# Kernel optimization log

Hardware: AMD Instinct MI355X
Metric: run time of the kernel (lower is better)

The kernel has to match this reference:

```python
import jax, jax.numpy as jnp
import numpy as np

HEADS, DIM_HEAD, LANDMARKS, PINV_ITERS = 8, 64, 256, 6


def moore_penrose_pinv(x, iters=PINV_ITERS):
    abs_x = jnp.abs(x)
    col = abs_x.sum(-1)
    row = abs_x.sum(-2)
    z = jnp.swapaxes(x, -1, -2) / (jnp.max(col) * jnp.max(row))
    I = jnp.eye(x.shape[-1], dtype=x.dtype)
    for _ in range(iters):
        xz = x @ z
        z = 0.25 * z @ (13 * I - xz @ (15 * I - xz @ (7 * I - xz)))
    return z


def nystrom_attention(x, w_qkv, w_out, b_out, res_conv_w):
    b, n, dim = x.shape
    m = LANDMARKS
    pad = (m - n % m) % m
    x = jnp.pad(x, ((0, 0), (pad, 0), (0, 0)))  # pad at front like F.pad(x,(0,0,pad,0))
    npad = n + pad
    qkv = x @ w_qkv  # (b, npad, 3*heads*dim_head)
    q, k, v = jnp.split(qkv, 3, axis=-1)
    sh = lambda t: t.reshape(b, npad, HEADS, DIM_HEAD).transpose(0, 2, 1, 3)
    q, k, v = sh(q), sh(k), sh(v)  # (b,h,npad,dh)
    q = q * (DIM_HEAD ** -0.5)
    l = npad // m
    q_l = q.reshape(b, HEADS, m, l, DIM_HEAD).mean(axis=3)  # landmarks (b,h,m,dh)
    k_l = k.reshape(b, HEADS, m, l, DIM_HEAD).mean(axis=3)
    attn1 = jax.nn.softmax(jnp.einsum('bhid,bhjd->bhij', q, k_l), -1)   # (b,h,npad,m)
    attn2 = jax.nn.softmax(jnp.einsum('bhid,bhjd->bhij', q_l, k_l), -1)  # (b,h,m,m)
    attn3 = jax.nn.softmax(jnp.einsum('bhid,bhjd->bhij', q_l, k), -1)   # (b,h,m,npad)
    out = attn1 @ (moore_penrose_pinv(attn2) @ (attn3 @ v))  # (b,h,npad,dh)
    # depthwise residual conv over sequence dim (Conv2d(heads,heads,(33,1),groups=heads,bias=False))
    res = jax.lax.conv_general_dilated(v, res_conv_w, (1, 1), ((16, 16), (0, 0)),
                                       dimension_numbers=('NCHW', 'OIHW', 'NCHW'),
                                       feature_group_count=HEADS)
    out = out + res
    out = out.transpose(0, 2, 1, 3).reshape(b, npad, HEADS * DIM_HEAD)
    out = out @ w_out + b_out
    return out[:, -n:]


def camil_forward(bag, adj_row, adj_col, adj_val, w_qkv, w_out, b_out, res_conv_w,
                  wq, wk, wv_w, wv_b, v_att, u_att, w_att, fc_kernel, fc_bias):
    N = bag.shape[1]
    # encoder
    xg = nystrom_attention(bag, w_qkv, w_out, b_out, res_conv_w)[0]  # (N,D)
    enc = xg + bag  # (1,N,D)
    q = enc @ wq  # (1,N,256)
    k = enc @ wk
    attn = jnp.einsum('bnd,bmd->bnm', q, k)[0] / jnp.sqrt(jnp.float32(256.0))  # (N,N)
    # sparse adjacency-masked neighbor aggregation
    edge_scores = adj_val * attn[adj_row, adj_col]
    A_raw = jax.ops.segment_sum(edge_scores, adj_row, num_segments=N)  # (N,)
    alpha = jax.nn.softmax(A_raw)
    value = bag @ wv_w + wv_b  # (1,N,D)
    xl = alpha[:, None] * value  # (1,N,D)
    wei2 = jax.nn.sigmoid(-xl) ** 2
    xo = xl * 2 * wei2 + 2 * enc * (1 - wei2)  # (1,N,D)
    # gated MIL attention (softmax over dim 0 of size 1, as in original)
    inst = jnp.tanh(xo @ v_att) * jax.nn.sigmoid(xo @ u_att)
    scores = inst @ w_att  # (1,N,1)
    k_alpha = jax.nn.softmax(scores, axis=0)
    attn_output = k_alpha * xo
    pooled = attn_output[0].sum(axis=0, keepdims=True)  # (1,D)
    out = pooled @ fc_kernel + fc_bias  # (1,1)
    return out, A_raw, k_alpha


def setup_inputs() -> dict:
    key = jax.random.key(0)
    ks = jax.random.split(key, 16)
    N, D, E = 10000, 512, 90000
    s = 0.02
    return {
        'bag': jax.random.normal(ks[0], (1, N, D), jnp.float32),
        'adj_row': jax.random.randint(ks[1], (E,), 0, N),
        'adj_col': jax.random.randint(ks[2], (E,), 0, N),
        'adj_val': jax.random.uniform(ks[3], (E,), jnp.float32),
        'w_qkv': jax.random.normal(ks[4], (D, 3 * HEADS * DIM_HEAD), jnp.float32) * s,
        'w_out': jax.random.normal(ks[5], (HEADS * DIM_HEAD, D), jnp.float32) * s,
        'b_out': jnp.zeros((D,), jnp.float32),
        'res_conv_w': jax.random.normal(ks[6], (HEADS, 1, 33, 1), jnp.float32) * s,
        'wq': jax.random.normal(ks[7], (D, 256), jnp.float32) * s,
        'wk': jax.random.normal(ks[8], (D, 256), jnp.float32) * s,
        'wv_w': jax.random.normal(ks[9], (D, D), jnp.float32) * s,
        'wv_b': jnp.zeros((D,), jnp.float32),
        'v_att': jax.random.normal(ks[10], (D, 128), jnp.float32) * s,
        'u_att': jax.random.normal(ks[11], (D, 128), jnp.float32) * s,
        'w_att': jax.random.normal(ks[12], (128, 1), jnp.float32) * s,
        'fc_kernel': jax.random.normal(ks[13], (D, 1), jnp.float32) * s,
        'fc_bias': jnp.zeros((1,), jnp.float32),
    }


def reference(bag, adj_row, adj_col, adj_val, w_qkv, w_out, b_out, res_conv_w,
              wq, wk, wv_w, wv_b, v_att, u_att, w_att, fc_kernel, fc_bias):
    return camil_forward(bag, adj_row, adj_col, adj_val, w_qkv, w_out, b_out, res_conv_w,
                         wq, wk, wv_w, wv_b, v_att, u_att, w_att, fc_kernel, fc_bias)
```

## Files before the change

### kernel.cpp

```cpp
#include <hip/hip_runtime.h>
#include <hip/hip_bf16.h>
#include <math.h>

#define NSEQ   10000
#define NPAD   10240
#define PADR   240
#define HEADS  8
#define DH     64
#define LM     256
#define LFAC   40
#define DMODEL 512
#define DQK    256
#define OUTSZ  20001
#define NSPLIT 16
#define KCH    128

typedef __attribute__((ext_vector_type(8))) short bf16x8;
typedef __attribute__((ext_vector_type(4))) float f32x4;
#define MFMA16(a,b,c) __builtin_amdgcn_mfma_f32_16x16x32_bf16(a,b,c,0,0,0)

typedef __attribute__((address_space(1))) const unsigned char gconst_t;
typedef __attribute__((address_space(3))) unsigned char lds_t;
#define GLD16(gp, lp) __builtin_amdgcn_global_load_lds((gconst_t*)(gp), (lds_t*)(lp), 16, 0, 0)

__device__ __forceinline__ float b2f(ushort u) {
    return __uint_as_float(((unsigned)u) << 16);
}
__device__ __forceinline__ ushort f2b(float f) {
    unsigned u = __float_as_uint(f);
    unsigned r = (u + 0x7FFFu + ((u >> 16) & 1u)) >> 16;
    return (ushort)r;
}
__device__ __forceinline__ int swz8(int bid, int nwg) {
    int q = nwg >> 3, r = nwg & 7;
    int x = bid & 7, idx = bid >> 3;
    int start = (x < r) ? x * (q + 1) : r * (q + 1) + (x - r) * q;
    return start + idx;
}
__device__ __forceinline__ f32x4 tr4(f32x4 v, int p) {
    f32x4 u, w;
    float s, r;
    s = (p & 1) ? v[0] : v[1]; r = __shfl_xor(s, 1);
    u[0] = (p & 1) ? r : v[0]; u[1] = (p & 1) ? v[1] : r;
    s = (p & 1) ? v[2] : v[3]; r = __shfl_xor(s, 1);
    u[2] = (p & 1) ? r : v[2]; u[3] = (p & 1) ? v[3] : r;
    s = (p & 2) ? u[0] : u[2]; r = __shfl_xor(s, 2);
    w[0] = (p & 2) ? r : u[0]; w[2] = (p & 2) ? u[2] : r;
    s = (p & 2) ? u[1] : u[3]; r = __shfl_xor(s, 2);
    w[1] = (p & 2) ? r : u[1]; w[3] = (p & 2) ? u[3] : r;
    return w;
}

__global__ __launch_bounds__(256)
void cvt_k(const float* __restrict__ in, ushort* __restrict__ out, int n4,
           float* __restrict__ outbuf, const float* __restrict__ fcb,
           unsigned int* __restrict__ mx)
{
    int i = blockIdx.x * 256 + threadIdx.x;
    if (i < n4) {
        float4 v = ((const float4*)in)[i];
        ushort4 u; u.x = f2b(v.x); u.y = f2b(v.y); u.z = f2b(v.z); u.w = f2b(v.w);
        ((ushort4*)out)[i] = u;
    }
    if (i == 0) { outbuf[0] = fcb[0]; mx[0] = 0u; mx[1] = 0u; }
    if (i >= 1 && i <= NSEQ) outbuf[i] = 0.f;
    if (i >= NSEQ + 1 && i < OUTSZ) outbuf[i] = 1.0f;
}

__global__ __launch_bounds__(256)
void wtrans_k(const float* __restrict__ w_qkv, const float* __restrict__ w_out,
              const float* __restrict__ wq, const float* __restrict__ wk,
              const float* __restrict__ wv_w,
              ushort* __restrict__ wqkvT, ushort* __restrict__ woutT,
              ushort* __restrict__ wqkT)
{
    __shared__ float tile[32][33];
    int g0 = blockIdx.x * 32, r0 = blockIdx.y * 32;
    const float* in; ushort* outp; int C; int lc0;
    if (g0 < 1536)      { in = w_qkv; outp = wqkvT;                      C = 1536; lc0 = g0; }
    else if (g0 < 2048) { in = w_out; outp = woutT;                      C = 512;  lc0 = g0 - 1536; }
    else if (g0 < 2304) { in = wq;    outp = wqkT;                       C = 256;  lc0 = g0 - 2048; }
    else if (g0 < 2560) { in = wk;    outp = wqkT + 256*512;             C = 256;  lc0 = g0 - 2304; }
    else                { in = wv_w;  outp = wqkvT + (size_t)1536*512;   C = 512;  lc0 = g0 - 2560; }
    int tx = threadIdx.x & 31, ty = threadIdx.x >> 5;
    for (int i = ty; i < 32; i += 8) tile[i][tx] = in[(size_t)(r0 + i) * C + lc0 + tx];
    __syncthreads();
    for (int i = ty; i < 32; i += 8) outp[(size_t)(lc0 + i) * 512 + r0 + tx] = f2b(tile[tx][i]);
}

template<int MODE, int TN>
__global__ __launch_bounds__(256)
void mgemm(const ushort* __restrict__ A, const ushort* __restrict__ Bt,
           int Mlog, int N, int K, int padr, int nbx,
           void* __restrict__ P0, void* __restrict__ P1, void* __restrict__ P2,
           void* __restrict__ P3, void* __restrict__ P4,
           const float* __restrict__ bias, const float* __restrict__ extra)
{
    constexpr int NF = TN / 32;
    __shared__ __align__(16) char As[128 * 64];
    __shared__ __align__(16) char Bs[TN * 64];
    const int tid = threadIdx.x;
    const int l = tid & 63, w = tid >> 6;
    const int wm = w >> 1, wn = w & 1;
    const int wk_ = swz8(blockIdx.x, gridDim.x);
    const int row0 = (wk_ / nbx) * 128, col0 = (wk_ % nbx) * TN;
    const int lr = l & 15, lg = l >> 4;
    const bool slow = (MODE == 0) && (row0 < padr);
    f32x4 acc[4][NF];
    #pragma unroll
    for (int i = 0; i < 4; ++i)
        #pragma unroll
        for (int j = 0; j < NF; ++j) acc[i][j] = (f32x4){0.f, 0.f, 0.f, 0.f};

    for (int k0 = 0; k0 < K; k0 += 32) {
        if (!slow) {
            #pragma unroll
            for (int c = 0; c < 2; ++c) {
                int q = w * 2 + c;
                int row = q * 16 + (l >> 2);
                GLD16(A + (size_t)(row0 + row - padr) * K + k0 + (l & 3) * 8,
                      As + q * 1024);
            }
            if (TN == 128) {
                #pragma unroll
                for (int c = 0; c < 2; ++c) {
                    int q = w * 2 + c;
                    int row = q * 16 + (l >> 2);
                    GLD16(Bt + (size_t)(col0 + row) * K + k0 + (l & 3) * 8,
                          Bs + q * 1024);
                }
            } else {
                int row = w * 16 + (l >> 2);
                GLD16(Bt + (size_t)(col0 + row) * K + k0 + (l & 3) * 8,
                      Bs + w * 1024);
            }
        } else {
            #pragma unroll
            for (int c = 0; c < 2; ++c) {
                int gidx = c * 256 + tid;
                int row = gidx >> 2, gr = gidx & 3;
                int phys = row0 + row - padr;
                uint4 v = {0, 0, 0, 0};
                if (phys >= 0 && phys < Mlog - padr)
                    v = *(const uint4*)(A + (size_t)phys * K + k0 + gr * 8);
                *(uint4*)(As + gidx * 16) = v;
            }
            if (TN == 128) {
                #pragma unroll
                for (int c = 0; c < 2; ++c) {
                    int gidx = c * 256 + tid;
                    int row = gidx >> 2, gr = gidx & 3;
                    *(uint4*)(Bs + gidx * 16) =
                        *(const uint4*)(Bt + (size_t)(col0 + row) * K + k0 + gr * 8);
                }
            } else {
                int row = tid >> 2, gr = tid & 3;
                *(uint4*)(Bs + tid * 16) =
                    *(const uint4*)(Bt + (size_t)(col0 + row) * K + k0 + gr * 8);
            }
        }
        __syncthreads();
        bf16x8 af[4];
        #pragma unroll
        for (int mf = 0; mf < 4; ++mf)
            af[mf] = *(const bf16x8*)(As + (wm * 64 + mf * 16 + lr) * 64 + lg * 16);
        #pragma unroll
        for (int nf = 0; nf < NF; ++nf) {
            bf16x8 bfr = *(const bf16x8*)(Bs + (wn * (TN / 2) + nf * 16 + lr) * 64 + lg * 16);
            #pragma unroll
            for (int mf = 0; mf < 4; ++mf)
                acc[mf][nf] = MFMA16(af[mf], bfr, acc[mf][nf]);
        }
        __syncthreads();
    }

    const int p = lr & 3;
    #pragma unroll
    for (int mf = 0; mf < 4; ++mf)
    #pragma unroll
    for (int nf = 0; nf < NF; ++nf) {
        int cb   = col0 + wn * (TN / 2) + nf * 16 + (lr & 12);
        int rowT = row0 + wm * 64 + mf * 16 + lg * 4 + p;
        if (MODE == 0) {
            int c = col0 + wn * (TN / 2) + nf * 16 + lr;
            if ((c >> 9) == 2) {
                int hh = (c >> 6) & 7;
                int kt  = (row0 + wm * 64 + mf * 16 + lg * 4) >> 5;
                int lgp = ((mf * 2) + (lg >> 1)) & 3;
                int lanep = lr + lgp * 16;
                int e0 = (lg & 1) * 4;
                ushort4 pk;
                pk.x = f2b(acc[mf][nf][0]); pk.y = f2b(acc[mf][nf][1]);
                pk.z = f2b(acc[mf][nf][2]); pk.w = f2b(acc[mf][nf][3]);
                *(ushort4*)&((ushort*)P3)[(((size_t)hh * (NPAD/32) + kt) * 4 + (nf & 3)) * 512
                                          + lanep * 8 + e0] = pk;
            }
            int t = cb >> 9;
            f32x4 v = acc[mf][nf];
            if (t == 0) { v[0] *= 0.125f; v[1] *= 0.125f; v[2] *= 0.125f; v[3] *= 0.125f; }
            f32x4 wv = tr4(v, p);
            ushort4 pk;
            pk.x = f2b(wv[0]); pk.y = f2b(wv[1]); pk.z = f2b(wv[2]); pk.w = f2b(wv[3]);
            if (t < 3) {
                int hh = (cb >> 6) & 7, d0 = cb & 63;
                ushort* dst = (t == 0) ? (ushort*)P0 : (t == 1) ? (ushort*)P1 : (ushort*)P2;
                *(ushort4*)&dst[((size_t)hh * NPAD + rowT) * DH + d0] = pk;
            } else {
                int phys = rowT - PADR;
                if (phys >= 0)
                    *(ushort4*)&((ushort*)P4)[(size_t)phys * DMODEL + (cb & 511)] = pk;
            }
        } else if (MODE == 1) {
            f32x4 wv = tr4(acc[mf][nf], p);
            if (rowT < Mlog) {
                float4 bi = *(const float4*)(bias + cb);
                float4 ex = *(const float4*)(extra + (size_t)rowT * N + cb);
                float o0 = wv[0] + bi.x + ex.x, o1 = wv[1] + bi.y + ex.y;
                float o2 = wv[2] + bi.z + ex.z, o3 = wv[3] + bi.w + ex.w;
                *(float4*)&((float*)P0)[(size_t)rowT * N + cb] = make_float4(o0, o1, o2, o3);
                ushort4 pk; pk.x = f2b(o0); pk.y = f2b(o1); pk.z = f2b(o2); pk.w = f2b(o3);
                *(ushort4*)&((ushort*)P1)[(size_t)rowT * N + cb] = pk;
            }
        } else if (MODE == 6) {
            f32x4 wv = tr4(acc[mf][nf], p);
            if (rowT < Mlog) {
                ushort4 pk;
                pk.x = f2b(wv[0]); pk.y = f2b(wv[1]); pk.z = f2b(wv[2]); pk.w = f2b(wv[3]);
                if (cb < 256)
                    *(ushort4*)&((ushort*)P0)[(size_t)rowT * 256 + cb] = pk;
                else
                    *(ushort4*)&((ushort*)P1)[(size_t)rowT * 256 + (cb - 256)] = pk;
            }
        }
    }
}

template<bool PLAIN, bool BCI, bool WPK>
__global__ __launch_bounds__(256)
void pinv_k(const ushort* __restrict__ A, const ushort* __restrict__ Bt,
            int N, float cval, float scale,
            ushort* __restrict__ P0, ushort* __restrict__ P1)
{
    __shared__ __align__(16) char smem[49152];
    char* As = smem;
    char* Bs = smem + 16384;
    const int tid = threadIdx.x, l = tid & 63, w = tid >> 6;
    const int lr = l & 15, lg = l >> 4;
    const int col0 = blockIdx.x * 64, row0 = blockIdx.y * 32, h = blockIdx.z;
    const ushort* Ab = A + (size_t)h * 65536;
    const ushort* Btb = Bt + (size_t)h * ((size_t)N * 256);
    {
        int row = tid >> 3, seg = (tid & 7) * 64;
        const uint4* sa = (const uint4*)(Ab + (size_t)(row0 + row) * 256) + (tid & 7) * 4;
        #pragma unroll
        for (int e = 0; e < 4; ++e) {
            int off = (row * 512 + seg + e * 16) ^ ((row & 7) << 4);
            *(uint4*)(As + off) = sa[e];
        }
    }
    {
        int row = tid >> 2, seg = (tid & 3) * 128;
        const uint4* sb = (const uint4*)(Btb + (size_t)(col0 + row) * 256) + (tid & 3) * 8;
        int gn = col0 + row;
        #pragma unroll
        for (int e = 0; e < 8; ++e) {
            int off = (row * 512 + seg + e * 16) ^ ((row & 7) << 4);
            uint4 vb = sb[e];
            if (BCI) {
                union { uint4 u; ushort s[8]; } t; t.u = vb;
                int gk0 = (seg >> 1) + e * 8;
                #pragma unroll
                for (int j = 0; j < 8; ++j)
                    t.s[j] = f2b(((gn == gk0 + j) ? cval : 0.f) - b2f(t.s[j]));
                vb = t.u;
            }
            *(uint4*)(Bs + off) = vb;
        }
    }
    __syncthreads();
    f32x4 acc[2];
    acc[0] = (f32x4){0.f, 0.f, 0.f, 0.f};
    acc[1] = (f32x4){0.f, 0.f, 0.f, 0.f};
    #pragma unroll
    for (int ks = 0; ks < 8; ++ks) {
        bf16x8 af[2];
        #pragma unroll
        for (int mf = 0; mf < 2; ++mf) {
            int ar = mf * 16 + lr;
            af[mf] = *(const bf16x8*)(As + ((ar * 512 + ks * 64 + lg * 16) ^ ((ar & 7) << 4)));
        }
        int br = w * 16 + lr;
        bf16x8 bf = *(const bf16x8*)(Bs + ((br * 512 + ks * 64 + lg * 16) ^ ((br & 7) << 4)));
        acc[0] = MFMA16(af[0], bf, acc[0]);
        acc[1] = MFMA16(af[1], bf, acc[1]);
    }
    #pragma unroll
    for (int mf = 0; mf < 2; ++mf) {
        int r0v = row0 + mf * 16 + lg * 4;
        int c = col0 + w * 16 + lr;
        if (PLAIN) {
            #pragma unroll
            for (int i = 0; i < 4; ++i)
                P0[(size_t)h * 256 * N + (size_t)(r0v + i) * N + c] = f2b(acc[mf][i] * scale);
        }
        ushort4 pk;
        pk.x = f2b(acc[mf][0] * scale); pk.y = f2b(acc[mf][1] * scale);
        pk.z = f2b(acc[mf][2] * scale); pk.w = f2b(acc[mf][3] * scale);
        if (WPK) {
            int off = (((c >> 4) * 8 + (r0v >> 5)) << 9) + (((r0v >> 3) & 3) << 7)
                    + ((c & 15) << 3) + (r0v & 4);
            *(ushort4*)&P1[(size_t)h * 16384 + off] = pk;
        } else {
            *(ushort4*)&P1[(size_t)h * ((size_t)N * 256) + (size_t)c * 256 + r0v] = pk;
        }
    }
}

__global__ void landmark2_k(const ushort* __restrict__ Qb, const ushort* __restrict__ Kb,
                            ushort* __restrict__ QLb, ushort* __restrict__ KLb,
                            ushort* __restrict__ KLpk)
{
    int b = blockIdx.x;
    bool isK = b >= HEADS * LM;
    if (isK) b -= HEADS * LM;
    int hh = b >> 8, j = b & 255, d = threadIdx.x;
    const ushort* p = (isK ? Kb : Qb) + ((size_t)hh * NPAD + (size_t)j * LFAC) * DH + d;
    float s = 0.f;
    #pragma unroll
    for (int t = 0; t < LFAC; ++t) s += b2f(p[t * DH]);
    ushort u = f2b(s * (1.f / LFAC));
    (isK ? KLb : QLb)[((size_t)hh * LM + j) * DH + d] = u;
    if (isK) {
        int nf = j >> 4, lr = j & 15;
        int ks = d >> 5, lg = (d >> 3) & 3, e = d & 7;
        KLpk[(((size_t)hh * 16 + nf) * 2 + ks) * 512 + (lg * 16 + lr) * 8 + e] = u;
    }
}

__global__ __launch_bounds__(256)
void attn2_k(const ushort* __restrict__ QL, const ushort* __restrict__ KL,
             ushort* __restrict__ X2b)
{
    int i = blockIdx.x, h = blockIdx.y, j = threadIdx.x;
    __shared__ float qv[DH];
    __shared__ float red[256];
    if (j < DH) qv[j] = b2f(QL[((size_t)h * LM + i) * DH + j]);
    __syncthreads();
    const uint4* kp = (const uint4*)(KL + ((size_t)h * LM + j) * DH);
    float dot = 0.f;
    #pragma unroll
    for (int cc = 0; cc < 8; ++cc) {
        union { uint4 u; ushort s[8]; } uu; uu.u = kp[cc];
        #pragma unroll
        for (int e = 0; e < 8; ++e) dot += qv[cc * 8 + e] * b2f(uu.s[e]);
    }
    red[j] = dot; __syncthreads();
    for (int s = 128; s > 0; s >>= 1) { if (j < s) red[j] = fmaxf(red[j], red[j + s]); __syncthreads(); }
    float mx = red[0]; __syncthreads();
    float e = __expf(dot - mx);
    red[j] = e; __syncthreads();
    for (int s = 128; s > 0; s >>= 1) { if (j < s) red[j] += red[j + s]; __syncthreads(); }
    X2b[((size_t)h * LM + i) * LM + j] = f2b(e / red[0]);
}

__global__ __launch_bounds__(256)
void colrow_k(const ushort* __restrict__ X2b, unsigned int* __restrict__ mx)
{
    int h = blockIdx.x, t = threadIdx.x;
    const ushort* x = X2b + (size_t)h * LM * LM;
    float cs = 0.f, rs = 0.f;
    for (int j = 0; j < LM; ++j) cs += fabsf(b2f(x[(size_t)t * LM + j]));
    for (int i = 0; i < LM; ++i) rs += fabsf(b2f(x[(size_t)i * LM + t]));
    __shared__ float r1[256], r2[256];
    r1[t] = cs; r2[t] = rs; __syncthreads();
    for (int s = 128; s > 0; s >>= 1) {
        if (t < s) { r1[t] = fmaxf(r1[t], r1[t + s]); r2[t] = fmaxf(r2[t], r2[t + s]); }
        __syncthreads();
    }
    if (t == 0) {
        atomicMax(&mx[0], __float_as_uint(r1[0]));
        atomicMax(&mx[1], __float_as_uint(r2[0]));
    }
}

__global__ void zinit_k(const ushort* __restrict__ X2b, const float* __restrict__ mxf,
                        ushort* __restrict__ Z, ushort* __restrict__ Zt)
{
    int i = blockIdx.x, h = blockIdx.y, j = threadIdx.x;
    float scale = 1.f / (mxf[0] * mxf[1]);
    float x = b2f(X2b[((size_t)h * LM + i) * LM + j]) * scale;
    ushort u = f2b(x);
    Z[((size_t)h * LM + j) * LM + i] = u;
    Zt[((size_t)h * LM + i) * LM + j] = u;
}

__global__ __launch_bounds__(256)
void attn3_fa(const ushort* __restrict__ QLb, const ushort* __restrict__ Kb,
              const ushort* __restrict__ VtPk,
              float* __restrict__ Opart, float* __restrict__ Mpart,
              float* __restrict__ Lpart)
{
    __shared__ __align__(16) char smem[9216 + 18432];
    ushort* Qs = (ushort*)smem;
    ushort* Ks = (ushort*)(smem + 9216);
    ushort* Ps = (ushort*)(smem + 9216);
    const int tid = threadIdx.x, l = tid & 63, wv = tid >> 6;
    const int split = blockIdx.x, qt = blockIdx.y, h = blockIdx.z;
    const int lr = l & 15, lg = l >> 4;
    {
        int row = tid >> 2, seg = (tid & 3) * 16;
        const uint4* src = (const uint4*)(QLb + ((size_t)h * LM + qt * 64 + row) * DH + seg);
        *(uint4*)&Qs[row * 72 + seg] = src[0];
        *(uint4*)&Qs[row * 72 + seg + 8] = src[1];
    }
    f32x4 o[4];
    float m_[4], l_[4];
    #pragma unroll
    for (int nf = 0; nf < 4; ++nf) o[nf] = (f32x4){0.f, 0.f, 0.f, 0.f};
    #pragma unroll
    for (int i = 0; i < 4; ++i) { m_[i] = -INFINITY; l_[i] = 0.f; }
    const int k0base = split * (NPAD / NSPLIT);
    for (int ch = 0; ch < NPAD / NSPLIT / KCH; ++ch) {
        int kg0 = k0base + ch * KCH;
        __syncthreads();
        {
            int row = tid >> 1, half = (tid & 1) * 32;
            const uint4* src = (const uint4*)(Kb + ((size_t)h * NPAD + kg0 + row) * DH + half);
            #pragma unroll
            for (int e = 0; e < 4; ++e) *(uint4*)&Ks[row * 72 + half + e * 8] = src[e];
        }
        __syncthreads();
        f32x4 s[8];
        #pragma unroll
        for (int nf = 0; nf < 8; ++nf) s[nf] = (f32x4){0.f, 0.f, 0.f, 0.f};
        #pragma unroll
        for (int ks = 0; ks < 2; ++ks) {
            bf16x8 a = *(const bf16x8*)&Qs[(wv * 16 + lr) * 72 + ks * 32 + lg * 8];
            #pragma unroll
            for (int nf = 0; nf < 8; ++nf) {
                bf16x8 b = *(const bf16x8*)&Ks[(nf * 16 + lr) * 72 + ks * 32 + lg * 8];
                s[nf] = MFMA16(a, b, s[nf]);
            }
        }
        float scl[4];
        #pragma unroll
        for (int i = 0; i < 4; ++i) {
            float mx = s[0][i];
            #pragma unroll
            for (int nf = 1; nf < 8; ++nf) mx = fmaxf(mx, s[nf][i]);
            mx = fmaxf(mx, __shfl_xor(mx, 1)); mx = fmaxf(mx, __shfl_xor(mx, 2));
            mx = fmaxf(mx, __shfl_xor(mx, 4)); mx = fmaxf(mx, __shfl_xor(mx, 8));
            float mn = fmaxf(m_[i], mx);
            float sum = 0.f;
            #pragma unroll
            for (int nf = 0; nf < 8; ++nf) {
                float e = __expf(s[nf][i] - mn); s[nf][i] = e; sum += e;
            }
            sum += __shfl_xor(sum, 1); sum += __shfl_xor(sum, 2);
            sum += __shfl_xor(sum, 4); sum += __shfl_xor(sum, 8);
            float sc = __expf(m_[i] - mn);
            l_[i] = l_[i] * sc + sum;
            m_[i] = mn;
            scl[i] = sc;
        }
        #pragma unroll
        for (int nf = 0; nf < 4; ++nf)
        #pragma unroll
        for (int i = 0; i < 4; ++i) o[nf][i] *= scl[i];
        __syncthreads();
        #pragma unroll
        for (int nf = 0; nf < 8; ++nf)
        #pragma unroll
        for (int i = 0; i < 4; ++i) {
            int row = wv * 16 + lg * 4 + i;
            int col = nf * 16 + lr;
            Ps[row * 128 + (col ^ ((row & 7) << 3))] = f2b(s[nf][i]);
        }
        #pragma unroll
        for (int ks = 0; ks < 4; ++ks) {
            int row = wv * 16 + lr;
            int kcol = ks * 32 + lg * 8;
            bf16x8 a = *(const bf16x8*)&Ps[row * 128 + (kcol ^ ((row & 7) << 3))];
            int kgt = (kg0 >> 5) + ks;
            #pragma unroll
            for (int nf = 0; nf < 4; ++nf) {
                bf16x8 b = *(const bf16x8*)(VtPk +
                    (((size_t)h * (NPAD/32) + kgt) * 4 + nf) * 512 + (size_t)l * 8);
                o[nf] = MFMA16(a, b, o[nf]);
            }
        }
    }
    const int base = (split * 4 + qt) * 8 + h;
    #pragma unroll
    for (int nf = 0; nf < 4; ++nf)
    #pragma unroll
    for (int i = 0; i < 4; ++i) {
        int r = wv * 16 + lg * 4 + i;
        int c = nf * 16 + lr;
        Opart[((size_t)base * 64 + r) * 64 + c] = o[nf][i];
    }
    if (lr == 0) {
        #pragma unroll
        for (int i = 0; i < 4; ++i) {
            int r = wv * 16 + lg * 4 + i;
            Mpart[base * 64 + r] = m_[i];
            Lpart[base * 64 + r] = l_[i];
        }
    }
}

__global__ __launch_bounds__(256)
void mergeAV_k(const float* __restrict__ Opart, const float* __restrict__ Mpart,
               const float* __restrict__ Lpart, ushort* __restrict__ AVt)
{
    int qt = blockIdx.x, h = blockIdx.y, rq = blockIdx.z;
    int t = threadIdx.x;
    int r = rq * 32 + (t >> 3), c0 = (t & 7) * 8;
    float mv[NSPLIT];
    float mstar = -INFINITY;
    #pragma unroll
    for (int s = 0; s < NSPLIT; ++s) {
        mv[s] = Mpart[((s * 4 + qt) * 8 + h) * 64 + r];
        mstar = fmaxf(mstar, mv[s]);
    }
    float wgt[NSPLIT];
    float L = 0.f;
    #pragma unroll
    for (int s = 0; s < NSPLIT; ++s) {
        wgt[s] = __expf(mv[s] - mstar);
        L += wgt[s] * Lpart[((s * 4 + qt) * 8 + h) * 64 + r];
    }
    float inv = 1.f / L;
    float acc[8] = {};
    #pragma unroll
    for (int s = 0; s < NSPLIT; ++s) {
        const float* op = Opart + (((size_t)(s * 4 + qt) * 8 + h) * 64 + r) * 64 + c0;
        #pragma unroll
        for (int e = 0; e < 8; ++e) acc[e] += wgt[s] * op[e];
    }
    #pragma unroll
    for (int e = 0; e < 8; ++e)
        AVt[((size_t)h * DH + c0 + e) * LM + qt * 64 + r] = f2b(acc[e] * inv);
}

__global__ __launch_bounds__(256)
void conv_k(const ushort* __restrict__ Vb, const float* __restrict__ cw,
            ushort* __restrict__ OBc)
{
    int idx = blockIdx.x * 256 + threadIdx.x;
    if (idx >= NSEQ * 128) return;
    int ro = idx >> 7, c4 = idx & 127;
    int h = c4 >> 4, dq = (c4 & 15) * 4;
    int i = ro + PADR;
    float a0 = 0, a1 = 0, a2 = 0, a3 = 0;
    #pragma unroll
    for (int tt = 0; tt < 33; ++tt) {
        int src = i + tt - 16;
        if (src < NPAD) {
            float wv = cw[h * 33 + tt];
            ushort4 u = *(const ushort4*)(Vb + ((size_t)h * NPAD + src) * DH + dq);
            a0 += wv * b2f(u.x); a1 += wv * b2f(u.y);
            a2 += wv * b2f(u.z); a3 += wv * b2f(u.w);
        }
    }
    ushort4 o; o.x = f2b(a0); o.y = f2b(a1); o.z = f2b(a2); o.w = f2b(a3);
    *(ushort4*)&OBc[(size_t)ro * DMODEL + h * DH + dq] = o;
}

__global__ __launch_bounds__(256, 4)
void outrows64v2(const ushort* __restrict__ Qb, const ushort* __restrict__ KLpk,
                 const ushort* __restrict__ Wpk, const ushort* __restrict__ OBc,
                 ushort* __restrict__ OBb)
{
    __shared__ __align__(16) char smem[40960];
    char*   Qs  = smem;
    ushort* KLs = (ushort*)(smem + 8192);
    ushort* Ps  = (ushort*)(smem + 8192);
    const int tid = threadIdx.x, l = tid & 63, w = tid >> 6;
    const int h = blockIdx.y, i0 = blockIdx.x * 64;
    const int lr = l & 15, lg = l >> 4;

    ushort obc[4][4];
    #pragma unroll
    for (int nf = 0; nf < 4; ++nf)
    #pragma unroll
    for (int i = 0; i < 4; ++i) {
        int r = i0 + w * 16 + lg * 4 + i;
        obc[nf][i] = (r >= PADR)
            ? OBc[(size_t)(r - PADR) * DMODEL + h * DH + nf * 16 + lr] : (ushort)0;
    }
    {
        int row = tid >> 2;
        int seg = (tid & 3) * 32;
        const uint4* src = (const uint4*)(Qb + ((size_t)h * NPAD + i0 + row) * DH) + (tid & 3) * 2;
        uint4 v0 = src[0], v1 = src[1];
        int sw = (row & 7) << 4;
        *(uint4*)(Qs + row * 128 + (seg ^ sw)) = v0;
        *(uint4*)(Qs + row * 128 + ((seg + 16) ^ sw)) = v1;
    }
    {
        const uint4* src = (const uint4*)(KLpk + (size_t)h * 16384) + tid;
        uint4* dst = (uint4*)KLs + tid;
        #pragma unroll
        for (int e = 0; e < 8; ++e) dst[e * 256] = src[e * 256];
    }
    __syncthreads();

    f32x4 s[16];
    #pragma unroll
    for (int nf = 0; nf < 16; ++nf) s[nf] = (f32x4){0.f, 0.f, 0.f, 0.f};
    #pragma unroll
    for (int ks = 0; ks < 2; ++ks) {
        int qrow = w * 16 + lr;
        bf16x8 a = *(const bf16x8*)(Qs + qrow * 128 +
                                    ((ks * 64 + lg * 16) ^ ((qrow & 7) << 4)));
        #pragma unroll
        for (int nf = 0; nf < 16; ++nf) {
            bf16x8 b = *(const bf16x8*)&KLs[((nf * 2 + ks) * 64 + l) * 8];
            s[nf] = MFMA16(a, b, s[nf]);
        }
    }
    float inv_[4];
    #pragma unroll
    for (int i = 0; i < 4; ++i) {
        float m = s[0][i];
        #pragma unroll
        for (int nf = 1; nf < 16; ++nf) m = fmaxf(m, s[nf][i]);
        m = fmaxf(m, __shfl_xor(m, 1)); m = fmaxf(m, __shfl_xor(m, 2));
        m = fmaxf(m, __shfl_xor(m, 4)); m = fmaxf(m, __shfl_xor(m, 8));
        float sum = 0.f;
        #pragma unroll
        for (int nf = 0; nf < 16; ++nf) {
            float e = __expf(s[nf][i] - m); s[nf][i] = e; sum += e;
        }
        sum += __shfl_xor(sum, 1); sum += __shfl_xor(sum, 2);
        sum += __shfl_xor(sum, 4); sum += __shfl_xor(sum, 8);
        inv_[i] = 1.f / sum;
    }
    __syncthreads();
    #pragma unroll
    for (int nf = 0; nf < 16; ++nf)
    #pragma unroll
    for (int i = 0; i < 4; ++i) {
        int row = w * 16 + lg * 4 + i;
        int col = nf * 16 + lr;
        Ps[row * 256 + (col ^ ((row & 7) << 3))] = f2b(s[nf][i] * inv_[i]);
    }
    f32x4 o[4];
    #pragma unroll
    for (int nf = 0; nf < 4; ++nf) o[nf] = (f32x4){0.f, 0.f, 0.f, 0.f};
    #pragma unroll
    for (int ks = 0; ks < 8; ++ks) {
        int row = w * 16 + lr;
        int kcol = ks * 32 + lg * 8;
        bf16x8 a = *(const bf16x8*)&Ps[row * 256 + (kcol ^ ((row & 7) << 3))];
        #pragma unroll
        for (int nf = 0; nf < 4; ++nf) {
            bf16x8 b = *(const bf16x8*)(Wpk + (((size_t)h * 2048) + nf * 512 + ks * 64 + l) * 8);
            o[nf] = MFMA16(a, b, o[nf]);
        }
    }
    #pragma unroll
    for (int nf = 0; nf < 4; ++nf)
    #pragma unroll
    for (int i = 0; i < 4; ++i) {
        int r = i0 + w * 16 + lg * 4 + i;
        if (r >= PADR) {
            int ro = r - PADR;
            int c = h * DH + nf * 16 + lr;
            OBb[(size_t)ro * DMODEL + c] = f2b(o[nf][i] + b2f(obc[nf][i]));
        }
    }
}

__global__ __launch_bounds__(256)
void edges_k(const int* __restrict__ rows, const int* __restrict__ cols,
             const float* __restrict__ vals,
             const ushort* __restrict__ QE, const ushort* __restrict__ KE,
             float* __restrict__ A_raw, int E)
{
    int gid = blockIdx.x * blockDim.x + threadIdx.x;
    int e = gid >> 4, l = gid & 15;
    if (e >= E) return;
    int r = rows[e], c = cols[e];
    const uint4* qp = (const uint4*)(QE + (size_t)r * DQK + l * 16);
    const uint4* kp = (const uint4*)(KE + (size_t)c * DQK + l * 16);
    float dot = 0.f;
    #pragma unroll
    for (int g = 0; g < 2; ++g) {
        union { uint4 u; ushort s[8]; } qq, kk;
        qq.u = qp[g]; kk.u = kp[g];
        #pragma unroll
        for (int j = 0; j < 8; ++j) dot += b2f(qq.s[j]) * b2f(kk.s[j]);
    }
    dot += __shfl_xor(dot, 8); dot += __shfl_xor(dot, 4);
    dot += __shfl_xor(dot, 2); dot += __shfl_xor(dot, 1);
    if (l == 0) atomicAdd(&A_raw[r], vals[e] * dot * 0.0625f);
}

__global__ __launch_bounds__(1024)
void alphasm_k(const float* __restrict__ A_raw, float* __restrict__ alpha)
{
    __shared__ float red[1024];
    int t = threadIdx.x;
    float lm = -INFINITY;
    for (int i = t; i < NSEQ; i += 1024) lm = fmaxf(lm, A_raw[i]);
    red[t] = lm; __syncthreads();
    for (int s = 512; s > 0; s >>= 1) { if (t < s) red[t] = fmaxf(red[t], red[t + s]); __syncthreads(); }
    float mx = red[0]; __syncthreads();
    float ls = 0.f;
    for (int i = t; i < NSEQ; i += 1024) ls += __expf(A_raw[i] - mx);
    red[t] = ls; __syncthreads();
    for (int s = 512; s > 0; s >>= 1) { if (t < s) red[t] += red[t + s]; __syncthreads(); }
    float inv = 1.f / red[0];
    for (int i = t; i < NSEQ; i += 1024) alpha[i] = __expf(A_raw[i] - mx) * inv;
}

__global__ __launch_bounds__(256)
void xo_pooled_k(const ushort* __restrict__ VALb, const float* __restrict__ ENCf,
                 const float* __restrict__ alpha, const float* __restrict__ wvb,
                 const float* __restrict__ fck, float* __restrict__ out0)
{
    __shared__ float red[256];
    int t = threadIdx.x;
    float acc = 0.f;
    const int total = NSEQ * 128;
    for (int idx = blockIdx.x * 256 + t; idx < total; idx += gridDim.x * 256) {
        int r = idx >> 7, dq = (idx & 127) * 4;
        float al = alpha[r];
        ushort4 v4 = *(const ushort4*)(VALb + (size_t)r * DMODEL + dq);
        float4 e4 = *(const float4*)(ENCf + (size_t)r * DMODEL + dq);
        float4 b4 = *(const float4*)(wvb + dq);
        float4 f4 = *(const float4*)(fck + dq);
        float vv[4] = {b2f(v4.x) + b4.x, b2f(v4.y) + b4.y,
                       b2f(v4.z) + b4.z, b2f(v4.w) + b4.w};
        float ee[4] = {e4.x, e4.y, e4.z, e4.w};
        float ff[4] = {f4.x, f4.y, f4.z, f4.w};
        #pragma unroll
        for (int j = 0; j < 4; ++j) {
            float xl = al * vv[j];
            float s = 1.f / (1.f + __expf(xl));
            float w2 = s * s;
            float xo = 2.f * xl * w2 + 2.f * ee[j] * (1.f - w2);
            acc += xo * ff[j];
        }
    }
    red[t] = acc; __syncthreads();
    for (int s = 128; s > 0; s >>= 1) { if (t < s) red[t] += red[t + s]; __syncthreads(); }
    if (t == 0) atomicAdd(out0, red[0]);
}

extern "C" void kernel_launch(void* const* d_in, const int* in_sizes, int n_in,
                              void* d_out, int out_size, void* d_ws, size_t ws_size,
                              hipStream_t stream)
{
    (void)n_in; (void)out_size; (void)ws_size;
    const float* bag   = (const float*)d_in[0];
    const int*   arow  = (const int*)d_in[1];
    const int*   acol  = (const int*)d_in[2];
    const float* aval  = (const float*)d_in[3];
    const float* w_qkv = (const float*)d_in[4];
    const float* w_out = (const float*)d_in[5];
    const float* b_out = (const float*)d_in[6];
    const float* convw = (const float*)d_in[7];
    const float* wq    = (const float*)d_in[8];
    const float* wk    = (const float*)d_in[9];
    const float* wv_w  = (const float*)d_in[10];
    const float* wv_b  = (const float*)d_in[11];
    const float* fck   = (const float*)d_in[15];
    const float* fcb   = (const float*)d_in[16];
    const int E = in_sizes[1];
    float* out = (float*)d_out;

    char* ws = (char*)d_ws;
    size_t off = 0;
    auto alloc = [&](size_t bytes) { void* p = ws + off; off += (bytes + 255) & ~(size_t)255; return p; };
    ushort* Qb    = (ushort*)alloc((size_t)HEADS * NPAD * DH * 2);
    ushort* Kb    = (ushort*)alloc((size_t)HEADS * NPAD * DH * 2);
    ushort* Vb    = (ushort*)alloc((size_t)HEADS * NPAD * DH * 2);
    ushort* bagb  = (ushort*)alloc((size_t)NSEQ * DMODEL * 2);
    ushort* wqkvT = (ushort*)alloc((size_t)2048 * 512 * 2);
    ushort* woutT = (ushort*)alloc((size_t)512 * 512 * 2);
    ushort* wqkT  = (ushort*)alloc((size_t)512 * 512 * 2);
    ushort* VALb  = (ushort*)alloc((size_t)NSEQ * DMODEL * 2);
    ushort* QLb   = (ushort*)alloc((size_t)HEADS * LM * DH * 2);
    ushort* KLb   = (ushort*)alloc((size_t)HEADS * LM * DH * 2);
    ushort* KLpk  = (ushort*)alloc((size_t)HEADS * LM * DH * 2);
    ushort* Wpk   = (ushort*)alloc((size_t)HEADS * DH * LM * 2);
    ushort* X2b   = (ushort*)alloc((size_t)HEADS * LM * LM * 2);
    ushort* Za    = (ushort*)alloc((size_t)HEADS * LM * LM * 2);
    ushort* Zat   = (ushort*)alloc((size_t)HEADS * LM * LM * 2);
    ushort* Zb2   = (ushort*)alloc((size_t)HEADS * LM * LM * 2);
    ushort* Zbt2  = (ushort*)alloc((size_t)HEADS * LM * LM * 2);
    ushort* T0    = (ushort*)alloc((size_t)HEADS * LM * LM * 2);
    ushort* T0t   = (ushort*)alloc((size_t)HEADS * LM * LM * 2);
    ushort* T1t   = (ushort*)alloc((size_t)HEADS * LM * LM * 2);
    ushort* T2t   = (ushort*)alloc((size_t)HEADS * LM * LM * 2);
    ushort* AVt   = (ushort*)alloc((size_t)HEADS * DH * LM * 2);
    ushort* OBc   = (ushort*)alloc((size_t)NSEQ * DMODEL * 2);
    ushort* OBb   = (ushort*)alloc((size_t)NSEQ * DMODEL * 2);
    float*  ENCf  = (float*)alloc((size_t)NSEQ * DMODEL * 4);
    ushort* ENCb  = (ushort*)alloc((size_t)NSEQ * DMODEL * 2);
    float*  ALPHA = (float*)alloc((size_t)NPAD * 4);
    float*  MXf   = (float*)alloc(256);
    unsigned int* MX = (unsigned int*)MXf;
    ushort* QEb = Qb;
    ushort* KEb = Kb;
    ushort* VtPk  = (ushort*)ENCf;
    float*  Opart = (float*)ENCb;
    float*  Mpart = (float*)((char*)ENCb + 8388608);
    float*  Lpart = (float*)((char*)ENCb + 8519680);

    cvt_k<<<(NSEQ * DMODEL / 4 + 255) / 256, 256, 0, stream>>>(
        bag, bagb, NSEQ * DMODEL / 4, out, fcb, MX);
    wtrans_k<<<dim3(96, 16), 256, 0, stream>>>(w_qkv, w_out, wq, wk, wv_w,
                                               wqkvT, woutT, wqkT);

    mgemm<0, 128><<<1280, 256, 0, stream>>>(
        bagb, wqkvT, NPAD, 2048, 512, PADR, 16,
        Qb, Kb, Vb, VtPk, VALb, nullptr, nullptr);

    landmark2_k<<<2 * HEADS * LM, DH, 0, stream>>>(Qb, Kb, QLb, KLb, KLpk);

    attn2_k<<<dim3(LM, HEADS), 256, 0, stream>>>(QLb, KLb, X2b);
    colrow_k<<<HEADS, 256, 0, stream>>>(X2b, MX);
    zinit_k<<<dim3(LM, HEADS), 256, 0, stream>>>(X2b, MXf, Za, Zat);

    ushort *Z = Za, *Zt = Zat, *Zn = Zb2, *Znt = Zbt2;
    for (int it = 0; it < 6; ++it) {
        pinv_k<true,  false, false><<<dim3(4, 8, HEADS), 256, 0, stream>>>(
            X2b, Zt, LM, 0.f, 1.f, T0, T0t);
        pinv_k<false, true,  false><<<dim3(4, 8, HEADS), 256, 0, stream>>>(
            T0, T0t, LM, 7.f, 1.f, nullptr, T1t);
        pinv_k<false, true,  false><<<dim3(4, 8, HEADS), 256, 0, stream>>>(
            T0, T1t, LM, 15.f, 1.f, nullptr, T2t);
        pinv_k<true,  true,  false><<<dim3(4, 8, HEADS), 256, 0, stream>>>(
            Z, T2t, LM, 13.f, 0.25f, Zn, Znt);
        ushort* t;
        t = Z; Z = Zn; Zn = t;
        t = Zt; Zt = Znt; Znt = t;
    }

    attn3_fa<<<dim3(NSPLIT, 4, HEADS), 256, 0, stream>>>(QLb, Kb, VtPk, Opart, Mpart, Lpart);
    mergeAV_k<<<dim3(4, HEADS, 2), 256, 0, stream>>>(Opart, Mpart, Lpart, AVt);
    pinv_k<false, false, true><<<dim3(1, 8, HEADS), 256, 0, stream>>>(
        Za, AVt, DH, 0.f, 1.f, nullptr, Wpk);

    conv_k<<<(NSEQ * 128 + 255) / 256, 256, 0, stream>>>(Vb, convw, OBc);
    outrows64v2<<<dim3(NPAD / 64, HEADS), 256, 0, stream>>>(Qb, KLpk, Wpk, OBc, OBb);

    mgemm<1, 64><<<632, 256, 0, stream>>>(
        OBb, woutT, NSEQ, DMODEL, 512, 0, 8,
        ENCf, ENCb, nullptr, nullptr, nullptr, b_out, bag);

    mgemm<6, 64><<<632, 256, 0, stream>>>(
        ENCb, wqkT, NSEQ, 512, 512, 0, 8,
        QEb, KEb, nullptr, nullptr, nullptr, nullptr, nullptr);

    edges_k<<<(E * 16 + 255) / 256, 256, 0, stream>>>(arow, acol, aval, QEb, KEb, out + 1, E);
    alphasm_k<<<1, 1024, 0, stream>>>(out + 1, ALPHA);

    xo_pooled_k<<<1280, 256, 0, stream>>>(VALb, ENCf, ALPHA, wv_b, fck, out);
}
```

Baseline: 356.0 us.

## Double-buffer LDS tiles in mgemm to overlap global loads with MFMA

Splits the K-loop tile loads into a stage function and ping-pongs between two LDS buffers. The next K-slice is prefetched while MFMAs run on the current one, and one of the two barriers per iteration is dropped. This is meant to hide global-load latency in the QKV and projection GEMMs. It doubles LDS use per block, which may lower occupancy. The slow path's synchronous register loads also now sit before the compute.

```diff
diff --git a/kernel.cpp b/kernel.cpp
--- a/kernel.cpp
+++ b/kernel.cpp
@@ -97,8 +97,9 @@
            const float* __restrict__ bias, const float* __restrict__ extra)
 {
     constexpr int NF = TN / 32;
-    __shared__ __align__(16) char As[128 * 64];
-    __shared__ __align__(16) char Bs[TN * 64];
+    constexpr int BSB = TN * 64;
+    __shared__ __align__(16) char As[2 * 8192];
+    __shared__ __align__(16) char Bs[2 * BSB];
     const int tid = threadIdx.x;
     const int l = tid & 63, w = tid >> 6;
     const int wm = w >> 1, wn = w & 1;
@@ -106,20 +107,22 @@
     const int row0 = (wk_ / nbx) * 128, col0 = (wk_ % nbx) * TN;
     const int lr = l & 15, lg = l >> 4;
     const bool slow = (MODE == 0) && (row0 < padr);
+    const int NT = K >> 5;
     f32x4 acc[4][NF];
     #pragma unroll
     for (int i = 0; i < 4; ++i)
         #pragma unroll
         for (int j = 0; j < NF; ++j) acc[i][j] = (f32x4){0.f, 0.f, 0.f, 0.f};
 
-    for (int k0 = 0; k0 < K; k0 += 32) {
+    auto stage = [&](int bf, int t) {
+        int k0 = t << 5;
         if (!slow) {
             #pragma unroll
             for (int c = 0; c < 2; ++c) {
                 int q = w * 2 + c;
                 int row = q * 16 + (l >> 2);
                 GLD16(A + (size_t)(row0 + row - padr) * K + k0 + (l & 3) * 8,
-                      As + q * 1024);
+                      As + bf * 8192 + q * 1024);
             }
             if (TN == 128) {
                 #pragma unroll
@@ -127,12 +130,12 @@
                     int q = w * 2 + c;
                     int row = q * 16 + (l >> 2);
                     GLD16(Bt + (size_t)(col0 + row) * K + k0 + (l & 3) * 8,
-                          Bs + q * 1024);
+                          Bs + bf * BSB + q * 1024);
                 }
             } else {
                 int row = w * 16 + (l >> 2);
                 GLD16(Bt + (size_t)(col0 + row) * K + k0 + (l & 3) * 8,
-                      Bs + w * 1024);
+                      Bs + bf * BSB + w * 1024);
             }
         } else {
             #pragma unroll
@@ -143,35 +146,44 @@
                 uint4 v = {0, 0, 0, 0};
                 if (phys >= 0 && phys < Mlog - padr)
                     v = *(const uint4*)(A + (size_t)phys * K + k0 + gr * 8);
-                *(uint4*)(As + gidx * 16) = v;
+                *(uint4*)(As + bf * 8192 + gidx * 16) = v;
             }
             if (TN == 128) {
                 #pragma unroll
                 for (int c = 0; c < 2; ++c) {
                     int gidx = c * 256 + tid;
                     int row = gidx >> 2, gr = gidx & 3;
-                    *(uint4*)(Bs + gidx * 16) =
+                    *(uint4*)(Bs + bf * BSB + gidx * 16) =
                         *(const uint4*)(Bt + (size_t)(col0 + row) * K + k0 + gr * 8);
                 }
             } else {
                 int row = tid >> 2, gr = tid & 3;
-                *(uint4*)(Bs + tid * 16) =
+                *(uint4*)(Bs + bf * BSB + tid * 16) =
                     *(const uint4*)(Bt + (size_t)(col0 + row) * K + k0 + gr * 8);
             }
         }
-        __syncthreads();
+    };
+
+    int cur = 0;
+    stage(0, 0);
+    __syncthreads();
+    for (int t = 0; t < NT; ++t) {
+        if (t + 1 < NT) stage(cur ^ 1, t + 1);
+        const char* Ab = As + cur * 8192;
+        const char* Bb = Bs + cur * BSB;
         bf16x8 af[4];
         #pragma unroll
         for (int mf = 0; mf < 4; ++mf)
-            af[mf] = *(const bf16x8*)(As + (wm * 64 + mf * 16 + lr) * 64 + lg * 16);
+            af[mf] = *(const bf16x8*)(Ab + (wm * 64 + mf * 16 + lr) * 64 + lg * 16);
         #pragma unroll
         for (int nf = 0; nf < NF; ++nf) {
-            bf16x8 bfr = *(const bf16x8*)(Bs + (wn * (TN / 2) + nf * 16 + lr) * 64 + lg * 16);
+            bf16x8 bfr = *(const bf16x8*)(Bb + (wn * (TN / 2) + nf * 16 + lr) * 64 + lg * 16);
             #pragma unroll
             for (int mf = 0; mf < 4; ++mf)
                 acc[mf][nf] = MFMA16(af[mf], bfr, acc[mf][nf]);
         }
         __syncthreads();
+        cur ^= 1;
     }
 
     const int p = lr & 3;
```

Measured after the change: 352.6 us, median of 2. About the same (-1.0%).
